# Optimization experiments

Hardware: AMD Instinct MI355X
Metric: run time of the kernel (lower is better)

## Reference

```python
import jax, jax.numpy as jnp
import numpy as np
import math

D_MODEL = 512
N_HEADS = 8
D_K = D_MODEL // N_HEADS
N_SAMPLES = 16
BETA = 1.0
SCALE = 1.0 / math.sqrt(D_K)
PROPOSAL_TEMP = 0.5


def setup_inputs() -> dict:
    key = jax.random.key(0)
    ks = jax.random.split(key, 9)
    B, S = 2, 512
    x = jax.random.normal(ks[0], (B, S, D_MODEL), dtype=jnp.float32)
    init = lambda k: jax.random.normal(k, (D_MODEL, D_MODEL), dtype=jnp.float32) * 0.02
    return {
        "x": x,
        "Wq": init(ks[1]), "bq": jnp.zeros((D_MODEL,), jnp.float32),
        "Wk": init(ks[2]), "bk": jnp.zeros((D_MODEL,), jnp.float32),
        "Wv": init(ks[3]), "bv": jnp.zeros((D_MODEL,), jnp.float32),
        "Wo": init(ks[4]), "bo": jnp.zeros((D_MODEL,), jnp.float32),
    }


def _importance_sampled_weights(scores):
    # scores: [B,H,S,S]. Replicates the per-row Python loop, fully vectorized.
    B, H, Sq, Sk = scores.shape
    target = jax.nn.softmax(scores * BETA, axis=-1)            # [B,H,Sq,Sk]
    # optimal proposal: 0.5*target + 0.5*uniform
    prop = PROPOSAL_TEMP * target + (1.0 - PROPOSAL_TEMP) / Sk
    R = B * H * Sq
    tf = target.reshape(R, Sk)
    pf = prop.reshape(R, Sk)
    # tsu_backend.sample_binary_layer(log(p/(1-p))) == Bernoulli(p) sampling
    s = jax.random.bernoulli(jax.random.key(42), pf[:, None, :], (R, N_SAMPLES, Sk))
    # importance weight = prod(target[sel]) / (prod(prop[sel]) * prod(1-prop[~sel]))
    pt = jnp.prod(jnp.where(s, tf[:, None, :], 1.0), axis=-1)                 # [R,N]
    pp = jnp.prod(jnp.where(s, pf[:, None, :], 1.0 - pf[:, None, :]), axis=-1)
    valid = (s.sum(-1) > 0) & (pp > 0)
    w = jnp.where(valid, pt / jnp.maximum(pp, 1e-38), 0.0)
    ws = w.sum(-1, keepdims=True)
    w = jnp.where(ws > 0, w / jnp.maximum(ws, 1e-38), 1.0 / N_SAMPLES)        # [R,N]
    wa = jnp.einsum('rn,rnk->rk', w, s.astype(jnp.float32))                   # [R,Sk]
    was = wa.sum(-1, keepdims=True)
    wa = jnp.where(was > 0, wa / jnp.maximum(was, 1e-38), 1.0 / Sk)
    return wa.reshape(B, H, Sq, Sk)


def reference(x, Wq, bq, Wk, bk, Wv, bv, Wo, bo):
    B, S, Dm = x.shape
    proj = lambda W, b: (x @ W + b).reshape(B, S, N_HEADS, D_K).transpose(0, 2, 1, 3)
    Q = proj(Wq, bq)  # [B,H,S,dk]
    K = proj(Wk, bk)
    V = proj(Wv, bv)
    scores = jnp.einsum('bhqd,bhkd->bhqk', Q, K) * SCALE
    # torch builds weights via torch.tensor(...) which detaches => constant w.r.t. params
    attn = jax.lax.stop_gradient(_importance_sampled_weights(scores))
    out = jnp.einsum('bhqk,bhkd->bhqd', attn, V)
    out = out.transpose(0, 2, 1, 3).reshape(B, S, Dm)
    return out @ Wo + bo
```

## Files before the change

### kernel.cpp

```cpp
#include <hip/hip_runtime.h>
#include <cstdint>
#include <cstddef>


#define ROTL(x, r) __builtin_rotateleft32((x), (r))

#define QR8(s)                                                                \
  x0[0]+=x1[0];x0[1]+=x1[1];x0[2]+=x1[2];x0[3]+=x1[3];                        \
  x0[4]+=x1[4];x0[5]+=x1[5];x0[6]+=x1[6];x0[7]+=x1[7];                        \
  x1[0]=ROTL(x1[0],s);x1[1]=ROTL(x1[1],s);x1[2]=ROTL(x1[2],s);                \
  x1[3]=ROTL(x1[3],s);x1[4]=ROTL(x1[4],s);x1[5]=ROTL(x1[5],s);                \
  x1[6]=ROTL(x1[6],s);x1[7]=ROTL(x1[7],s);                                    \
  x1[0]^=x0[0];x1[1]^=x0[1];x1[2]^=x0[2];x1[3]^=x0[3];                        \
  x1[4]^=x0[4];x1[5]^=x0[5];x1[6]^=x0[6];x1[7]^=x0[7];
#define INJ8(X, Y)                                                            \
  x0[0]+=(X);x0[1]+=(X);x0[2]+=(X);x0[3]+=(X);                                \
  x0[4]+=(X);x0[5]+=(X);x0[6]+=(X);x0[7]+=(X);                                \
  x1[0]+=(Y);x1[1]+=(Y);x1[2]+=(Y);x1[3]+=(Y);                                \
  x1[4]+=(Y);x1[5]+=(Y);x1[6]+=(Y);x1[7]+=(Y);
#define INJ8Y(Y)                                                              \
  x1[0]+=(Y);x1[1]+=(Y);x1[2]+=(Y);x1[3]+=(Y);                                \
  x1[4]+=(Y);x1[5]+=(Y);x1[6]+=(Y);x1[7]+=(Y);

__global__ __launch_bounds__(256)
void qkv_gemm(const float* __restrict__ x,
              const float* __restrict__ Wq, const float* __restrict__ bq,
              const float* __restrict__ Wk, const float* __restrict__ bk,
              const float* __restrict__ Wv, const float* __restrict__ bv,
              const float* __restrict__ bo, float* __restrict__ outp,
              float* __restrict__ Qw, float* __restrict__ KTw,
              float* __restrict__ Vw) {
  const int tid = threadIdx.x;
  if (blockIdx.z == 3) {
    const int blk = blockIdx.y * 32 + blockIdx.x;
    const size_t base4 = (size_t)blk * 512 + tid;
    const float4* bo4 = (const float4*)bo;
    float4* out4 = (float4*)outp;
    out4[base4] = bo4[base4 & 127];
    out4[base4 + 256] = bo4[(base4 + 256) & 127];
    return;
  }
  const float* W; const float* bias;
  if (blockIdx.z == 0)      { W = Wq; bias = bq; }
  else if (blockIdx.z == 1) { W = Wk; bias = bk; }
  else                      { W = Wv; bias = bv; }

  __shared__ __align__(16) float smem[2 * (32 * 34 + 32 * 64)];
  float (*At0)[34] = (float(*)[34])smem;
  float (*Bs0)[64] = (float(*)[64])(smem + 32 * 34);
  float (*At1)[34] = (float(*)[34])(smem + 3136);
  float (*Bs1)[64] = (float(*)[64])(smem + 3136 + 32 * 34);
  float (*T2)[34]  = (float(*)[34])smem;

  const int tx = tid & 15, ty = tid >> 4;
  const int row0 = blockIdx.x * 32, col0 = blockIdx.y * 64;
  float acc[2][4] = {};

  const int ar = tid >> 3;
  const int kc = (tid & 7) << 2;
  const int br0 = tid >> 4,         bc0 = (tid & 15) << 2;
  const int br1 = (tid + 256) >> 4, bc1 = ((tid + 256) & 15) << 2;

  float4 aR, bR0, bR1;
  aR  = *(const float4*)&x[(size_t)(row0 + ar) * 512 + kc];
  bR0 = *(const float4*)&W[(size_t)br0 * 512 + col0 + bc0];
  bR1 = *(const float4*)&W[(size_t)br1 * 512 + col0 + bc1];

  At0[kc + 0][ar] = aR.x; At0[kc + 1][ar] = aR.y;
  At0[kc + 2][ar] = aR.z; At0[kc + 3][ar] = aR.w;
  *(float4*)&Bs0[br0][bc0] = bR0;
  *(float4*)&Bs0[br1][bc1] = bR1;
  __syncthreads();

  float (*Atc)[34] = At0; float (*Bsc)[64] = Bs0;
  float (*Atn)[34] = At1; float (*Bsn)[64] = Bs1;

  for (int kk = 0; kk < 512; kk += 32) {
    if (kk < 480) {
      const int kn = kk + 32;
      aR  = *(const float4*)&x[(size_t)(row0 + ar) * 512 + kn + kc];
      bR0 = *(const float4*)&W[(size_t)(kn + br0) * 512 + col0 + bc0];
      bR1 = *(const float4*)&W[(size_t)(kn + br1) * 512 + col0 + bc1];
    }
#pragma unroll
    for (int p = 0; p < 32; ++p) {
      const float2 a2 = *(const float2*)&Atc[p][ty << 1];
      const float4 b4 = *(const float4*)&Bsc[p][tx << 2];
      acc[0][0] = fmaf(a2.x, b4.x, acc[0][0]); acc[0][1] = fmaf(a2.x, b4.y, acc[0][1]);
      acc[0][2] = fmaf(a2.x, b4.z, acc[0][2]); acc[0][3] = fmaf(a2.x, b4.w, acc[0][3]);
      acc[1][0] = fmaf(a2.y, b4.x, acc[1][0]); acc[1][1] = fmaf(a2.y, b4.y, acc[1][1]);
      acc[1][2] = fmaf(a2.y, b4.z, acc[1][2]); acc[1][3] = fmaf(a2.y, b4.w, acc[1][3]);
    }
    if (kk < 480) {
      Atn[kc + 0][ar] = aR.x; Atn[kc + 1][ar] = aR.y;
      Atn[kc + 2][ar] = aR.z; Atn[kc + 3][ar] = aR.w;
      *(float4*)&Bsn[br0][bc0] = bR0;
      *(float4*)&Bsn[br1][bc1] = bR1;
    }
    __syncthreads();
    float (*tA)[34] = Atc; Atc = Atn; Atn = tA;
    float (*tB)[64] = Bsc; Bsc = Bsn; Bsn = tB;
  }

  const int h = blockIdx.y;
  if (blockIdx.z == 0 || blockIdx.z == 2) {
    float* dst = (blockIdx.z == 0) ? Qw : Vw;
#pragma unroll
    for (int i = 0; i < 2; ++i) {
      const int row = row0 + (ty << 1) + i;
      const int b = row >> 9, s = row & 511;
#pragma unroll
      for (int j = 0; j < 4; ++j) {
        const int col = col0 + (tx << 2) + j;
        const int d = col & 63;
        dst[(((size_t)(b * 8 + h) * 512 + s) * 64) + d] = acc[i][j] + bias[col];
      }
    }
  } else {
#pragma unroll
    for (int i = 0; i < 2; ++i) {
#pragma unroll
      for (int j = 0; j < 4; ++j) {
        const int col = col0 + (tx << 2) + j;
        T2[(tx << 2) + j][(ty << 1) + i] = acc[i][j] + bias[col];
      }
    }
    __syncthreads();
    const int b = row0 >> 9;
    const int s0 = row0 & 511;
#pragma unroll
    for (int i2 = 0; i2 < 2; ++i2) {
      const int idx = tid + (i2 << 8);
      const int c = idx >> 3, seg = idx & 7;
      float* dst = KTw + (((size_t)(b * 8 + h) * 64 + c) << 9) + s0 + (seg << 2);
      *(float4*)dst = *(const float4*)&T2[c][seg << 2];
    }
  }
}

__global__ __launch_bounds__(256)
void fused_sample(const float* __restrict__ Q, const float* __restrict__ KT,
                  const float* __restrict__ V, const float* __restrict__ Wo,
                  float* __restrict__ outp) {
  const int bx = blockIdx.x;
  const int rbase = ((((bx & 7) << 8) | (bx >> 3)) << 2);
  const int bh = rbase >> 9, q0 = rbase & 511;
  const int b = rbase >> 12, h = (rbase >> 9) & 7;
  const int tid = threadIdx.x;

  __shared__ __align__(16) float qs[4][64];
  __shared__ __align__(16) float scs[4][512];
  __shared__ float red[8];
  __shared__ float redc[8];
  __shared__ float wr[16];
  __shared__ float tf[512];
  __shared__ __align__(16) uint32_t pscu2[512];
  __shared__ float wa[512];
  __shared__ float psum[4][64];
  __shared__ __align__(16) float o_s[4][64];
  __shared__ int   list[512];
  __shared__ int   cnt;

  qs[tid >> 6][tid & 63] =
      Q[((size_t)bh * 512 + q0 + (tid >> 6)) * 64 + (tid & 63)];
  __syncthreads();

  {
    const float* Kp = KT + (size_t)bh * 64 * 512 + tid;
    float s00 = 0.f, s01 = 0.f, s10 = 0.f, s11 = 0.f;
    float s20 = 0.f, s21 = 0.f, s30 = 0.f, s31 = 0.f;
#pragma unroll
    for (int d4 = 0; d4 < 16; ++d4) {
      float k0v[4], k1v[4];
#pragma unroll
      for (int j = 0; j < 4; ++j) {
        k0v[j] = Kp[(size_t)(d4 * 4 + j) * 512];
        k1v[j] = Kp[(size_t)(d4 * 4 + j) * 512 + 256];
      }
      const float4 q0v = *(const float4*)&qs[0][d4 << 2];
      const float4 q1v = *(const float4*)&qs[1][d4 << 2];
      const float4 q2v = *(const float4*)&qs[2][d4 << 2];
      const float4 q3v = *(const float4*)&qs[3][d4 << 2];
      s00 = fmaf(q0v.x, k0v[0], s00); s00 = fmaf(q0v.y, k0v[1], s00);
      s00 = fmaf(q0v.z, k0v[2], s00); s00 = fmaf(q0v.w, k0v[3], s00);
      s01 = fmaf(q0v.x, k1v[0], s01); s01 = fmaf(q0v.y, k1v[1], s01);
      s01 = fmaf(q0v.z, k1v[2], s01); s01 = fmaf(q0v.w, k1v[3], s01);
      s10 = fmaf(q1v.x, k0v[0], s10); s10 = fmaf(q1v.y, k0v[1], s10);
      s10 = fmaf(q1v.z, k0v[2], s10); s10 = fmaf(q1v.w, k0v[3], s10);
      s11 = fmaf(q1v.x, k1v[0], s11); s11 = fmaf(q1v.y, k1v[1], s11);
      s11 = fmaf(q1v.z, k1v[2], s11); s11 = fmaf(q1v.w, k1v[3], s11);
      s20 = fmaf(q2v.x, k0v[0], s20); s20 = fmaf(q2v.y, k0v[1], s20);
      s20 = fmaf(q2v.z, k0v[2], s20); s20 = fmaf(q2v.w, k0v[3], s20);
      s21 = fmaf(q2v.x, k1v[0], s21); s21 = fmaf(q2v.y, k1v[1], s21);
      s21 = fmaf(q2v.z, k1v[2], s21); s21 = fmaf(q2v.w, k1v[3], s21);
      s30 = fmaf(q3v.x, k0v[0], s30); s30 = fmaf(q3v.y, k0v[1], s30);
      s30 = fmaf(q3v.z, k0v[2], s30); s30 = fmaf(q3v.w, k0v[3], s30);
      s31 = fmaf(q3v.x, k1v[0], s31); s31 = fmaf(q3v.y, k1v[1], s31);
      s31 = fmaf(q3v.z, k1v[2], s31); s31 = fmaf(q3v.w, k1v[3], s31);
    }
    scs[0][tid] = s00 * 0.125f; scs[0][tid + 256] = s01 * 0.125f;
    scs[1][tid] = s10 * 0.125f; scs[1][tid + 256] = s11 * 0.125f;
    scs[2][tid] = s20 * 0.125f; scs[2][tid + 256] = s21 * 0.125f;
    scs[3][tid] = s30 * 0.125f; scs[3][tid + 256] = s31 * 0.125f;
  }

  const int n = tid >> 4, t = tid & 15;
  const int k0i = t << 5;
  const int g = tid >> 6, d = tid & 63;
  const float* Vb = V + ((size_t)(b * 8 + h) * 512) * 64;

  for (int rr = 0; rr < 4; ++rr) {
    const int r = rbase + rr;
    const float sc0 = scs[rr][tid];
    const float sc1 = scs[rr][tid + 256];

    float mx = fmaxf(sc0, sc1);
    for (int m = 1; m < 64; m <<= 1) mx = fmaxf(mx, __shfl_xor(mx, m));
    if ((tid & 63) == 0) red[tid >> 6] = mx;
    __syncthreads();
    const float rowmax = fmaxf(fmaxf(red[0], red[1]), fmaxf(red[2], red[3]));
    const float e0 = expf(sc0 - rowmax);
    const float e1 = expf(sc1 - rowmax);
    float ssum = e0 + e1;
    for (int m = 1; m < 64; m <<= 1) ssum += __shfl_xor(ssum, m);
    if ((tid & 63) == 0) red[4 + (tid >> 6)] = ssum;
    if (tid == 0) cnt = 0;
    __syncthreads();
    const float tot = red[4] + red[5] + red[6] + red[7];
    const float t0 = e0 / tot, t1 = e1 / tot;
    tf[tid] = t0; tf[tid + 256] = t1;
    wa[tid] = 0.f; wa[tid + 256] = 0.f;
    {
      const float p0 = fmaf(0.5f, t0, 0.0009765625f);
      const float p1 = fmaf(0.5f, t1, 0.0009765625f);
      {
        const int k = tid;
        pscu2[(((k & 31) >> 2) << 6) + ((k >> 5) << 2) + (k & 3)] =
            ((uint32_t)ceilf(p0 * 8388608.0f)) << 9;
      }
      {
        const int k = tid + 256;
        pscu2[(((k & 31) >> 2) << 6) + ((k >> 5) << 2) + (k & 3)] =
            ((uint32_t)ceilf(p1 * 8388608.0f)) << 9;
      }
      float ql = (1.f - p0) * (1.f - p1);
      for (int m = 1; m < 64; m <<= 1) ql *= __shfl_xor(ql, m);
      if ((tid & 63) == 0) redc[4 + (tid >> 6)] = ql;
    }
    __syncthreads();
    const float Qrow = redc[4] * redc[5] * redc[6] * redc[7];

    const uint32_t cbase =
        (uint32_t)r * 8192u + (uint32_t)n * 512u + (uint32_t)k0i + 42u;
    uint32_t bits = 0u;
#pragma unroll
    for (int jb = 0; jb < 32; jb += 8) {
      uint32_t x0[8], x1[8];
#pragma unroll
      for (int i = 0; i < 8; ++i) {
        const uint32_t c = cbase + (uint32_t)(jb + i);
        x0[i] = c;
        x1[i] = ROTL(c, 13) ^ c;
      }
      QR8(15) QR8(26) QR8(6)
      INJ8(42u, 0x1BD11BF1u)
      QR8(17) QR8(29) QR8(16) QR8(24)
      INJ8(0x1BD11BF0u, 2u)
      QR8(13) QR8(15) QR8(26) QR8(6)
      INJ8Y(45u)
      QR8(17) QR8(29) QR8(16) QR8(24)
      INJ8(42u, 0x1BD11BF4u)
      QR8(13) QR8(15) QR8(26) QR8(6)
      INJ8(0x1BD11BF0u, 5u)
      const uint4 pA = *(const uint4*)&pscu2[((jb >> 2) << 6) + (t << 2)];
      const uint4 pB = *(const uint4*)&pscu2[(((jb >> 2) + 1) << 6) + (t << 2)];
      bits |= (uint32_t)((x0[0] ^ x1[0]) < pA.x) << (jb + 0);
      bits |= (uint32_t)((x0[1] ^ x1[1]) < pA.y) << (jb + 1);
      bits |= (uint32_t)((x0[2] ^ x1[2]) < pA.z) << (jb + 2);
      bits |= (uint32_t)((x0[3] ^ x1[3]) < pA.w) << (jb + 3);
      bits |= (uint32_t)((x0[4] ^ x1[4]) < pB.x) << (jb + 4);
      bits |= (uint32_t)((x0[5] ^ x1[5]) < pB.y) << (jb + 5);
      bits |= (uint32_t)((x0[6] ^ x1[6]) < pB.z) << (jb + 6);
      bits |= (uint32_t)((x0[7] ^ x1[7]) < pB.w) << (jb + 7);
    }

    float ptl = 1.f, ratl = 1.f;
    int cl = __popc(bits);
    {
      uint32_t bb = bits;
      while (bb) {
        const int j = __builtin_ctz(bb);
        bb &= bb - 1u;
        const float tv = tf[k0i + j];
        const float p = fmaf(0.5f, tv, 0.0009765625f);
        ptl *= tv;
        ratl *= p / (1.f - p);
      }
    }
#pragma unroll
    for (int m = 1; m < 16; m <<= 1) {
      ptl *= __shfl_xor(ptl, m);
      ratl *= __shfl_xor(ratl, m);
      cl += __shfl_xor(cl, m);
    }
    if (t == 0) {
      const float pp = Qrow * ratl;
      wr[n] = (cl > 0 && pp > 0.f) ? (ptl / fmaxf(pp, 1e-38f)) : 0.f;
    }
    __syncthreads();
    float wsum = 0.f;
#pragma unroll
    for (int m2 = 0; m2 < 16; ++m2) wsum += wr[m2];
    const float wn = (wsum > 0.f) ? (wr[n] / fmaxf(wsum, 1e-38f)) : 0.0625f;
    {
      uint32_t bb = bits;
      while (bb) {
        const int j = __builtin_ctz(bb);
        bb &= bb - 1u;
        atomicAdd(&wa[k0i + j], wn);
      }
    }
    __syncthreads();

    float sp = wa[tid] + wa[tid + 256];
    for (int m = 1; m < 64; m <<= 1) sp += __shfl_xor(sp, m);
    if ((tid & 63) == 0) redc[tid >> 6] = sp;
    if (wa[tid] > 0.f)       { const int i = atomicAdd(&cnt, 1); list[i] = tid; }
    if (wa[tid + 256] > 0.f) { const int i = atomicAdd(&cnt, 1); list[i] = tid + 256; }
    __syncthreads();
    const float was = redc[0] + redc[1] + redc[2] + redc[3];
    const int nnz = cnt;

    float acc = 0.f;
    if (was > 0.f) {
      const float inv = 1.f / fmaxf(was, 1e-38f);
      for (int i = g; i < nnz; i += 4) {
        const int k = list[i];
        acc = fmaf(wa[k] * inv, Vb[(size_t)k * 64 + d], acc);
      }
    } else {
      for (int k = g; k < 512; k += 4) acc += Vb[(size_t)k * 64 + d];
      acc *= 0.001953125f;
    }
    psum[g][d] = acc;
    __syncthreads();
    if (g == 0)
      o_s[rr][d] = psum[0][d] + psum[1][d] + psum[2][d] + psum[3][d];
  }
  __syncthreads();

  {
    const float* Wh = Wo + ((size_t)h * 64) * 512;
    float a00 = 0.f, a01 = 0.f, a10 = 0.f, a11 = 0.f;
    float a20 = 0.f, a21 = 0.f, a30 = 0.f, a31 = 0.f;
#pragma unroll 8
    for (int dd = 0; dd < 64; ++dd) {
      const float w0 = Wh[(size_t)dd * 512 + tid];
      const float w1 = Wh[(size_t)dd * 512 + tid + 256];
      const float o0 = o_s[0][dd], o1 = o_s[1][dd];
      const float o2 = o_s[2][dd], o3 = o_s[3][dd];
      a00 = fmaf(o0, w0, a00); a01 = fmaf(o0, w1, a01);
      a10 = fmaf(o1, w0, a10); a11 = fmaf(o1, w1, a11);
      a20 = fmaf(o2, w0, a20); a21 = fmaf(o2, w1, a21);
      a30 = fmaf(o3, w0, a30); a31 = fmaf(o3, w1, a31);
    }
    float* orow = outp + ((size_t)(b * 512 + q0)) * 512;
    atomicAdd(&orow[tid], a00);         atomicAdd(&orow[tid + 256], a01);
    atomicAdd(&orow[512 + tid], a10);   atomicAdd(&orow[512 + tid + 256], a11);
    atomicAdd(&orow[1024 + tid], a20);  atomicAdd(&orow[1024 + tid + 256], a21);
    atomicAdd(&orow[1536 + tid], a30);  atomicAdd(&orow[1536 + tid + 256], a31);
  }
}

extern "C" void kernel_launch(void* const* d_in, const int* in_sizes, int n_in,
                              void* d_out, int out_size, void* d_ws,
                              size_t ws_size, hipStream_t stream) {
  const float* x  = (const float*)d_in[0];
  const float* Wq = (const float*)d_in[1];
  const float* bq = (const float*)d_in[2];
  const float* Wk = (const float*)d_in[3];
  const float* bk = (const float*)d_in[4];
  const float* Wv = (const float*)d_in[5];
  const float* bv = (const float*)d_in[6];
  const float* Wo = (const float*)d_in[7];
  const float* bo = (const float*)d_in[8];
  float* out = (float*)d_out;

  float* ws = (float*)d_ws;
  float* Qw = ws;
  float* KT = ws + 524288;
  float* Vw = ws + 1048576;

  dim3 gq(32, 8, 4);
  qkv_gemm<<<gq, 256, 0, stream>>>(x, Wq, bq, Wk, bk, Wv, bv, bo, out,
                                   Qw, KT, Vw);
  fused_sample<<<2048, 256, 0, stream>>>(Qw, KT, Vw, Wo, out);
}
```

Before: 252.4 us.

## Batch four rows per phase to cut barriers and split PV per wave

The fused sampling kernel used to handle its four query rows one after another, with about seven block barriers per row. It now runs each phase (softmax max, sum, proposal thresholds, Bernoulli sampling, weight scatter) across all four rows before a single barrier, keeping per-row state in larger shared arrays. The attention-times-V step gives one wave per row and uses a ballot over the nonzero weights, which replaces the atomic list build and the cross-wave partial-sum reduction. In exchange, each thread holds more registers and shared memory per block grows, which could lower occupancy.

```diff
diff --git a/kernel.cpp b/kernel.cpp
--- a/kernel.cpp
+++ b/kernel.cpp
@@ -147,22 +147,17 @@
   const int bh = rbase >> 9, q0 = rbase & 511;
   const int b = rbase >> 12, h = (rbase >> 9) & 7;
   const int tid = threadIdx.x;
-
-  __shared__ __align__(16) float qs[4][64];
-  __shared__ __align__(16) float scs[4][512];
-  __shared__ float red[8];
-  __shared__ float redc[8];
-  __shared__ float wr[16];
-  __shared__ float tf[512];
-  __shared__ __align__(16) uint32_t pscu2[512];
-  __shared__ float wa[512];
-  __shared__ float psum[4][64];
-  __shared__ __align__(16) float o_s[4][64];
-  __shared__ int   list[512];
-  __shared__ int   cnt;
-
-  qs[tid >> 6][tid & 63] =
-      Q[((size_t)bh * 512 + q0 + (tid >> 6)) * 64 + (tid & 63)];
+  const int w = tid >> 6, l = tid & 63;
+
+  __shared__ __align__(16) float    qs[4][64];
+  __shared__ __align__(16) float    tfs[4][512];
+  __shared__ __align__(16) uint32_t pscu[4][512];
+  __shared__ __align__(16) uint32_t bitsS[4][256];
+  __shared__ float redA[4][4], redB[4][4], redQ[4][4], redS[4][4];
+  __shared__ float wr[4][16];
+  __shared__ __align__(16) float o_sT[64][4];
+
+  qs[w][l] = Q[((size_t)bh * 512 + q0 + w) * 64 + l];
   __syncthreads();
 
   {
@@ -198,60 +193,67 @@
       s31 = fmaf(q3v.x, k1v[0], s31); s31 = fmaf(q3v.y, k1v[1], s31);
       s31 = fmaf(q3v.z, k1v[2], s31); s31 = fmaf(q3v.w, k1v[3], s31);
     }
-    scs[0][tid] = s00 * 0.125f; scs[0][tid + 256] = s01 * 0.125f;
-    scs[1][tid] = s10 * 0.125f; scs[1][tid + 256] = s11 * 0.125f;
-    scs[2][tid] = s20 * 0.125f; scs[2][tid + 256] = s21 * 0.125f;
-    scs[3][tid] = s30 * 0.125f; scs[3][tid + 256] = s31 * 0.125f;
-  }
+    tfs[0][tid] = s00 * 0.125f; tfs[0][tid + 256] = s01 * 0.125f;
+    tfs[1][tid] = s10 * 0.125f; tfs[1][tid + 256] = s11 * 0.125f;
+    tfs[2][tid] = s20 * 0.125f; tfs[2][tid + 256] = s21 * 0.125f;
+    tfs[3][tid] = s30 * 0.125f; tfs[3][tid + 256] = s31 * 0.125f;
+  }
+
+  float scA[4], scB[4];
+#pragma unroll
+  for (int rr = 0; rr < 4; ++rr) {
+    scA[rr] = tfs[rr][tid];
+    scB[rr] = tfs[rr][tid + 256];
+    float mx = fmaxf(scA[rr], scB[rr]);
+    for (int m = 1; m < 64; m <<= 1) mx = fmaxf(mx, __shfl_xor(mx, m));
+    if ((tid & 63) == 0) redA[rr][tid >> 6] = mx;
+  }
+  __syncthreads();
+
+  float e0v[4], e1v[4];
+#pragma unroll
+  for (int rr = 0; rr < 4; ++rr) {
+    const float rowmax = fmaxf(fmaxf(redA[rr][0], redA[rr][1]),
+                               fmaxf(redA[rr][2], redA[rr][3]));
+    e0v[rr] = expf(scA[rr] - rowmax);
+    e1v[rr] = expf(scB[rr] - rowmax);
+    float ssum = e0v[rr] + e1v[rr];
+    for (int m = 1; m < 64; m <<= 1) ssum += __shfl_xor(ssum, m);
+    if ((tid & 63) == 0) redB[rr][tid >> 6] = ssum;
+  }
+  __syncthreads();
+
+#pragma unroll
+  for (int rr = 0; rr < 4; ++rr) {
+    const float tot = redB[rr][0] + redB[rr][1] + redB[rr][2] + redB[rr][3];
+    const float t0 = e0v[rr] / tot, t1 = e1v[rr] / tot;
+    tfs[rr][tid] = t0; tfs[rr][tid + 256] = t1;
+    const float p0 = fmaf(0.5f, t0, 0.0009765625f);
+    const float p1 = fmaf(0.5f, t1, 0.0009765625f);
+    {
+      const int k = tid;
+      pscu[rr][(((k & 31) >> 2) << 6) + ((k >> 5) << 2) + (k & 3)] =
+          ((uint32_t)ceilf(p0 * 8388608.0f)) << 9;
+    }
+    {
+      const int k = tid + 256;
+      pscu[rr][(((k & 31) >> 2) << 6) + ((k >> 5) << 2) + (k & 3)] =
+          ((uint32_t)ceilf(p1 * 8388608.0f)) << 9;
+    }
+    float ql = (1.f - p0) * (1.f - p1);
+    for (int m = 1; m < 64; m <<= 1) ql *= __shfl_xor(ql, m);
+    if ((tid & 63) == 0) redQ[rr][tid >> 6] = ql;
+  }
+  __syncthreads();
 
   const int n = tid >> 4, t = tid & 15;
   const int k0i = t << 5;
-  const int g = tid >> 6, d = tid & 63;
-  const float* Vb = V + ((size_t)(b * 8 + h) * 512) * 64;
-
-  for (int rr = 0; rr < 4; ++rr) {
-    const int r = rbase + rr;
-    const float sc0 = scs[rr][tid];
-    const float sc1 = scs[rr][tid + 256];
-
-    float mx = fmaxf(sc0, sc1);
-    for (int m = 1; m < 64; m <<= 1) mx = fmaxf(mx, __shfl_xor(mx, m));
-    if ((tid & 63) == 0) red[tid >> 6] = mx;
-    __syncthreads();
-    const float rowmax = fmaxf(fmaxf(red[0], red[1]), fmaxf(red[2], red[3]));
-    const float e0 = expf(sc0 - rowmax);
-    const float e1 = expf(sc1 - rowmax);
-    float ssum = e0 + e1;
-    for (int m = 1; m < 64; m <<= 1) ssum += __shfl_xor(ssum, m);
-    if ((tid & 63) == 0) red[4 + (tid >> 6)] = ssum;
-    if (tid == 0) cnt = 0;
-    __syncthreads();
-    const float tot = red[4] + red[5] + red[6] + red[7];
-    const float t0 = e0 / tot, t1 = e1 / tot;
-    tf[tid] = t0; tf[tid + 256] = t1;
-    wa[tid] = 0.f; wa[tid + 256] = 0.f;
-    {
-      const float p0 = fmaf(0.5f, t0, 0.0009765625f);
-      const float p1 = fmaf(0.5f, t1, 0.0009765625f);
-      {
-        const int k = tid;
-        pscu2[(((k & 31) >> 2) << 6) + ((k >> 5) << 2) + (k & 3)] =
-            ((uint32_t)ceilf(p0 * 8388608.0f)) << 9;
-      }
-      {
-        const int k = tid + 256;
-        pscu2[(((k & 31) >> 2) << 6) + ((k >> 5) << 2) + (k & 3)] =
-            ((uint32_t)ceilf(p1 * 8388608.0f)) << 9;
-      }
-      float ql = (1.f - p0) * (1.f - p1);
-      for (int m = 1; m < 64; m <<= 1) ql *= __shfl_xor(ql, m);
-      if ((tid & 63) == 0) redc[4 + (tid >> 6)] = ql;
-    }
-    __syncthreads();
-    const float Qrow = redc[4] * redc[5] * redc[6] * redc[7];
-
-    const uint32_t cbase =
-        (uint32_t)r * 8192u + (uint32_t)n * 512u + (uint32_t)k0i + 42u;
+  for (int rr = 0; rr < 4; ++rr) {
+    const float Qrow = redQ[rr][0] * redQ[rr][1] * redQ[rr][2] * redQ[rr][3];
+    const uint32_t cbase = (uint32_t)(rbase + rr) * 8192u +
+                           (uint32_t)n * 512u + (uint32_t)k0i + 42u;
+    const uint32_t* psc = pscu[rr];
+    const float* tf = tfs[rr];
     uint32_t bits = 0u;
 #pragma unroll
     for (int jb = 0; jb < 32; jb += 8) {
@@ -272,8 +274,8 @@
       INJ8(42u, 0x1BD11BF4u)
       QR8(13) QR8(15) QR8(26) QR8(6)
       INJ8(0x1BD11BF0u, 5u)
-      const uint4 pA = *(const uint4*)&pscu2[((jb >> 2) << 6) + (t << 2)];
-      const uint4 pB = *(const uint4*)&pscu2[(((jb >> 2) + 1) << 6) + (t << 2)];
+      const uint4 pA = *(const uint4*)&psc[((jb >> 2) << 6) + (t << 2)];
+      const uint4 pB = *(const uint4*)&psc[(((jb >> 2) + 1) << 6) + (t << 2)];
       bits |= (uint32_t)((x0[0] ^ x1[0]) < pA.x) << (jb + 0);
       bits |= (uint32_t)((x0[1] ^ x1[1]) < pA.y) << (jb + 1);
       bits |= (uint32_t)((x0[2] ^ x1[2]) < pA.z) << (jb + 2);
@@ -283,6 +285,7 @@
       bits |= (uint32_t)((x0[6] ^ x1[6]) < pB.z) << (jb + 6);
       bits |= (uint32_t)((x0[7] ^ x1[7]) < pB.w) << (jb + 7);
     }
+    bitsS[rr][tid] = bits;
 
     float ptl = 1.f, ratl = 1.f;
     int cl = __popc(bits);
@@ -305,47 +308,65 @@
     }
     if (t == 0) {
       const float pp = Qrow * ratl;
-      wr[n] = (cl > 0 && pp > 0.f) ? (ptl / fmaxf(pp, 1e-38f)) : 0.f;
-    }
-    __syncthreads();
+      wr[rr][n] = (cl > 0 && pp > 0.f) ? (ptl / fmaxf(pp, 1e-38f)) : 0.f;
+    }
+  }
+  __syncthreads();
+
+  float* waf = (float*)pscu;
+  {
+    const float4 z4 = make_float4(0.f, 0.f, 0.f, 0.f);
+    ((float4*)waf)[tid] = z4;
+    ((float4*)waf)[tid + 256] = z4;
+  }
+  __syncthreads();
+
+  for (int rr = 0; rr < 4; ++rr) {
     float wsum = 0.f;
 #pragma unroll
-    for (int m2 = 0; m2 < 16; ++m2) wsum += wr[m2];
-    const float wn = (wsum > 0.f) ? (wr[n] / fmaxf(wsum, 1e-38f)) : 0.0625f;
-    {
-      uint32_t bb = bits;
-      while (bb) {
-        const int j = __builtin_ctz(bb);
-        bb &= bb - 1u;
-        atomicAdd(&wa[k0i + j], wn);
-      }
-    }
-    __syncthreads();
-
-    float sp = wa[tid] + wa[tid + 256];
+    for (int m2 = 0; m2 < 16; ++m2) wsum += wr[rr][m2];
+    const float wn = (wsum > 0.f) ? (wr[rr][n] / fmaxf(wsum, 1e-38f)) : 0.0625f;
+    float* war = waf + (rr << 9);
+    uint32_t bb = bitsS[rr][tid];
+    while (bb) {
+      const int j = __builtin_ctz(bb);
+      bb &= bb - 1u;
+      atomicAdd(&war[k0i + j], wn);
+    }
+  }
+  __syncthreads();
+
+#pragma unroll
+  for (int rr = 0; rr < 4; ++rr) {
+    float sp = waf[(rr << 9) + tid] + waf[(rr << 9) + tid + 256];
     for (int m = 1; m < 64; m <<= 1) sp += __shfl_xor(sp, m);
-    if ((tid & 63) == 0) redc[tid >> 6] = sp;
-    if (wa[tid] > 0.f)       { const int i = atomicAdd(&cnt, 1); list[i] = tid; }
-    if (wa[tid + 256] > 0.f) { const int i = atomicAdd(&cnt, 1); list[i] = tid + 256; }
-    __syncthreads();
-    const float was = redc[0] + redc[1] + redc[2] + redc[3];
-    const int nnz = cnt;
-
-    float acc = 0.f;
+    if ((tid & 63) == 0) redS[rr][tid >> 6] = sp;
+  }
+  __syncthreads();
+
+  {
+    const float was = redS[w][0] + redS[w][1] + redS[w][2] + redS[w][3];
+    const float* Vb = V + ((size_t)(b * 8 + h) * 512) * 64;
+    const float* war = waf + (w << 9);
+    float o = 0.f;
     if (was > 0.f) {
       const float inv = 1.f / fmaxf(was, 1e-38f);
-      for (int i = g; i < nnz; i += 4) {
-        const int k = list[i];
-        acc = fmaf(wa[k] * inv, Vb[(size_t)k * 64 + d], acc);
+#pragma unroll 1
+      for (int c = 0; c < 8; ++c) {
+        const float v = war[(c << 6) + l];
+        unsigned long long mask = __ballot(v > 0.f);
+        while (mask) {
+          const int j = __builtin_ctzll(mask);
+          mask &= mask - 1ull;
+          const int k = (c << 6) + j;
+          o = fmaf(war[k] * inv, Vb[(size_t)k * 64 + l], o);
+        }
       }
     } else {
-      for (int k = g; k < 512; k += 4) acc += Vb[(size_t)k * 64 + d];
-      acc *= 0.001953125f;
-    }
-    psum[g][d] = acc;
-    __syncthreads();
-    if (g == 0)
-      o_s[rr][d] = psum[0][d] + psum[1][d] + psum[2][d] + psum[3][d];
+      for (int k = 0; k < 512; ++k) o += Vb[(size_t)k * 64 + l];
+      o *= 0.001953125f;
+    }
+    o_sT[l][w] = o;
   }
   __syncthreads();
 
@@ -355,14 +376,13 @@
     float a20 = 0.f, a21 = 0.f, a30 = 0.f, a31 = 0.f;
 #pragma unroll 8
     for (int dd = 0; dd < 64; ++dd) {
+      const float4 o4 = *(const float4*)&o_sT[dd][0];
       const float w0 = Wh[(size_t)dd * 512 + tid];
       const float w1 = Wh[(size_t)dd * 512 + tid + 256];
-      const float o0 = o_s[0][dd], o1 = o_s[1][dd];
-      const float o2 = o_s[2][dd], o3 = o_s[3][dd];
-      a00 = fmaf(o0, w0, a00); a01 = fmaf(o0, w1, a01);
-      a10 = fmaf(o1, w0, a10); a11 = fmaf(o1, w1, a11);
-      a20 = fmaf(o2, w0, a20); a21 = fmaf(o2, w1, a21);
-      a30 = fmaf(o3, w0, a30); a31 = fmaf(o3, w1, a31);
+      a00 = fmaf(o4.x, w0, a00); a01 = fmaf(o4.x, w1, a01);
+      a10 = fmaf(o4.y, w0, a10); a11 = fmaf(o4.y, w1, a11);
+      a20 = fmaf(o4.z, w0, a20); a21 = fmaf(o4.z, w1, a21);
+      a30 = fmaf(o4.w, w0, a30); a31 = fmaf(o4.w, w1, a31);
     }
     float* orow = outp + ((size_t)(b * 512 + q0)) * 512;
     atomicAdd(&orow[tid], a00);         atomicAdd(&orow[tid + 256], a01);
```

Measured after the change: 251.4 us. No clear change (-0.4%).
